# Optimization experiments

Hardware: AMD Instinct MI355X
Metric: run time of the kernel (lower is better)

## Reference

```python
import jax, jax.numpy as jnp
import numpy as np

N_NODES = 30000
N_EDGES = 480000
N_GRAPHS = 512
NUM_NEIGHBORS = 3.8
DIM_SH = 16       # l=0..3 spherical harmonics
DIM_GATE_IN = 160 # 16x0e+16x0o + 8x0e+8x0o+8x0e+8x0o + 16x1o+16x1e
DIM_GATE_OUT = 128
DIM_OUT = 7       # 0o + 6x0e


def spherical_harmonics_l3(u):
    # real spherical harmonics l=0..3, 'component' normalization (|Y_l|^2 ~ 2l+1)
    x, y, z = u[:, 0], u[:, 1], u[:, 2]
    x2, y2, z2 = x * x, y * y, z * z
    sh = [
        jnp.ones_like(x),
        3 ** 0.5 * x, 3 ** 0.5 * y, 3 ** 0.5 * z,
        15 ** 0.5 * x * y, 15 ** 0.5 * y * z,
        (5 ** 0.5 / 2) * (3 * z2 - 1),
        15 ** 0.5 * x * z,
        (15 ** 0.5 / 2) * (x2 - y2),
        (35 / 8) ** 0.5 * y * (3 * x2 - y2),
        105 ** 0.5 * x * y * z,
        (21 / 8) ** 0.5 * y * (5 * z2 - 1),
        (7 ** 0.5 / 2) * z * (5 * z2 - 3),
        (21 / 8) ** 0.5 * x * (5 * z2 - 1),
        (105 ** 0.5 / 2) * z * (x2 - y2),
        (35 / 8) ** 0.5 * x * (x2 - y2),
    ]
    return jnp.stack(sh, axis=-1)  # [E, 16]


def radial_embed(r):
    # soft_one_hot_linspace(start=0.5, end=2.5, number=3, basis='smooth_finite', cutoff=True) * sqrt(3)
    values = jnp.array([0.5, 1.5, 2.5], dtype=r.dtype)
    u = r[:, None] - values          # step = 1.0
    d = u * u - 1.0
    c = 1.14136 * np.exp(2.0)
    emb = jnp.where(d < 0, c * jnp.exp(1.0 / jnp.where(d < 0, d, -1.0)), 0.0)
    return emb * 3 ** 0.5            # [E, 3]


def mlp(s, W1, W2):
    # FullyConnectedNet([3, 256, K], relu): no bias, fan-in normalized
    h = jax.nn.relu(s @ (W1 / 3 ** 0.5))
    return h @ (W2 / 256 ** 0.5)


def conv(nf, edge_src, edge_dst, sh, w, cg, n_nodes):
    # gather -> per-edge weighted CG bilinear product -> scatter-add
    xs = nf[edge_src]                      # [E, Din]
    K, Din, Dsh = cg.shape
    E = xs.shape[0]
    if Din * Dsh <= 512:
        outer = (xs[:, :, None] * sh[:, None, :]).reshape(E, Din * Dsh)
        ef = outer @ cg.reshape(K, Din * Dsh).T           # [E, K]
    else:
        t = jnp.einsum('ei,kij->ekj', xs, cg)             # [E, K, Dsh] (K small)
        ef = jnp.einsum('ekj,ej->ek', t, sh)
    ef = ef * w                                           # per-edge learned weights
    out = jax.ops.segment_sum(ef, edge_dst, num_segments=n_nodes)
    return out / NUM_NEIGHBORS ** 0.5


def gate(x):
    # Gate('16x0e+16x0o', [relu, abs], '8x0e+8x0o+8x0e+8x0o', [relu,tanh,relu,tanh], '16x1o+16x1e')
    n = x.shape[0]
    s = jnp.concatenate([jax.nn.relu(x[:, :16]), jnp.abs(x[:, 16:32])], axis=1)
    g = jnp.concatenate([
        jax.nn.relu(x[:, 32:40]), jnp.tanh(x[:, 40:48]),
        jax.nn.relu(x[:, 48:56]), jnp.tanh(x[:, 56:64]),
    ], axis=1)                                            # [n, 32]
    vec = x[:, 64:160].reshape(n, 32, 3)                  # 16x1o + 16x1e
    gated = (vec * g[:, :, None]).reshape(n, 96)
    return jnp.concatenate([s, gated], axis=1)            # [n, 128]


def setup_inputs() -> dict:
    key = jax.random.key(0)
    ks = jax.random.split(key, 10)
    pos = jax.random.normal(ks[0], (N_NODES, 3), dtype=jnp.float32)
    edge_src = jax.random.randint(ks[1], (N_EDGES,), 0, N_NODES)
    edge_dst = jax.random.randint(ks[2], (N_EDGES,), 0, N_NODES)
    batch = jnp.sort(jax.random.randint(ks[3], (N_NODES,), 0, N_GRAPHS))
    W1a = jax.random.normal(ks[4], (3, 256), dtype=jnp.float32)
    W2a = jax.random.normal(ks[5], (256, DIM_GATE_IN), dtype=jnp.float32)
    cg1 = jax.random.normal(ks[6], (DIM_GATE_IN, DIM_SH, DIM_SH), dtype=jnp.float32) / DIM_SH
    W1b = jax.random.normal(ks[7], (3, 256), dtype=jnp.float32)
    W2b = jax.random.normal(ks[8], (256, DIM_OUT), dtype=jnp.float32)
    cg2 = jax.random.normal(ks[9], (DIM_OUT, DIM_GATE_OUT, DIM_SH), dtype=jnp.float32) / DIM_SH
    return {"pos": pos, "W1a": W1a, "W2a": W2a, "cg1": cg1, "W1b": W1b,
            "W2b": W2b, "cg2": cg2, "edge_src": edge_src, "edge_dst": edge_dst,
            "batch": batch}


def reference(pos, W1a, W2a, cg1, W1b, W2b, cg2, edge_src, edge_dst, batch):
    ev = pos[edge_src] - pos[edge_dst]                    # [E, 3]
    r = jnp.linalg.norm(ev, axis=1)
    u = ev / jnp.maximum(r, 1e-9)[:, None]
    sh = spherical_harmonics_l3(u)                        # [E, 16]
    scal = radial_embed(r)                                # [E, 3]

    # initial node features: scatter of edge attributes
    x = jax.ops.segment_sum(sh, edge_dst, num_segments=N_NODES) / NUM_NEIGHBORS ** 0.5

    w1 = mlp(scal, W1a, W2a)                              # [E, 160]
    x = conv(x, edge_src, edge_dst, sh, w1, cg1, N_NODES) # [N, 160]
    x = gate(x)                                           # [N, 128]
    w2 = mlp(scal, W1b, W2b)                              # [E, 7]
    x = conv(x, edge_src, edge_dst, sh, w2, cg2, N_NODES) # [N, 7]

    out = jax.ops.segment_sum(x, batch, num_segments=N_GRAPHS) / 4 ** 0.5
    return out                                            # [512, 7]
```

## Files before the change

### kernel.cpp

```cpp
#include <hip/hip_runtime.h>
#include <math.h>

#define NN 30000
#define NE 480000
#define NG 512

#define INV_SQRT_NN 0.5129891760425771f
#define INV_SQRT3   0.5773502691896258f
#define SCALE_W2    0.0625f
#define RAD_C       14.607377f

typedef __bf16 bf16x8 __attribute__((ext_vector_type(8)));
typedef float f32x4 __attribute__((ext_vector_type(4)));
typedef unsigned short ushort8 __attribute__((ext_vector_type(8)));

__device__ __forceinline__ unsigned short f2bf(float f) {
  unsigned int u = __float_as_uint(f);
  return (unsigned short)((u + 0x7FFFu + ((u >> 16) & 1u)) >> 16);
}

__global__ __launch_bounds__(256) void k_edge(
    const float* __restrict__ pos,
    const int* __restrict__ esrc,
    const int* __restrict__ edst,
    float* __restrict__ shg,
    float* __restrict__ scalg,
    float* __restrict__ x0) {
  __shared__ float S_lds[256*17];
  __shared__ int   d_lds[256];
  const int t = threadIdx.x;
  const int e = blockIdx.x * 256 + t;
  int s = esrc[e], d = edst[e];
  float ex = pos[3*s]   - pos[3*d];
  float ey = pos[3*s+1] - pos[3*d+1];
  float ez = pos[3*s+2] - pos[3*d+2];
  float r = sqrtf(ex*ex + ey*ey + ez*ez);
  float inv = 1.0f / fmaxf(r, 1e-9f);
  float x = ex*inv, y = ey*inv, z = ez*inv;
  float x2 = x*x, y2 = y*y, z2 = z*z;
  float S[16];
  S[0]  = 1.0f;
  S[1]  = 1.7320508075688772f * x;
  S[2]  = 1.7320508075688772f * y;
  S[3]  = 1.7320508075688772f * z;
  S[4]  = 3.872983346207417f * x * y;
  S[5]  = 3.872983346207417f * y * z;
  S[6]  = 1.118033988749895f * (3.0f*z2 - 1.0f);
  S[7]  = 3.872983346207417f * x * z;
  S[8]  = 1.9364916731037085f * (x2 - y2);
  S[9]  = 2.091650066335189f  * y * (3.0f*x2 - y2);
  S[10] = 10.246950765959598f * x * y * z;
  S[11] = 1.6201851746019651f * y * (5.0f*z2 - 1.0f);
  S[12] = 1.3228756555322954f * z * (5.0f*z2 - 3.0f);
  S[13] = 1.6201851746019651f * x * (5.0f*z2 - 1.0f);
  S[14] = 5.123475382979799f  * z * (x2 - y2);
  S[15] = 2.091650066335189f  * x * (x2 - y2);
  float4* shv = (float4*)(shg + (size_t)e * 16);
  shv[0] = make_float4(S[0],  S[1],  S[2],  S[3]);
  shv[1] = make_float4(S[4],  S[5],  S[6],  S[7]);
  shv[2] = make_float4(S[8],  S[9],  S[10], S[11]);
  shv[3] = make_float4(S[12], S[13], S[14], S[15]);
  float sc[3];
  #pragma unroll
  for (int c = 0; c < 3; ++c) {
    float v = 0.5f + (float)c;
    float uu = r - v;
    float dd = uu*uu - 1.0f;
    sc[c] = (dd < 0.0f) ? RAD_C * expf(1.0f/dd) : 0.0f;
  }
  ((float4*)scalg)[e] = make_float4(sc[0], sc[1], sc[2], 0.0f);

  d_lds[t] = d;
  #pragma unroll
  for (int j = 0; j < 16; ++j) S_lds[t*17 + j] = S[j];
  __syncthreads();
  #pragma unroll
  for (int it = 0; it < 16; ++it) {
    int idx = it*256 + t;
    int el = idx >> 4, j = idx & 15;
    atomicAdd(&x0[(size_t)d_lds[el]*16 + j], S_lds[el*17 + j]);
  }
}

__global__ void k_prep(const float* __restrict__ W2a, const float* __restrict__ cg1,
                       const float* __restrict__ cg2, const float* __restrict__ W2b,
                       unsigned short* __restrict__ Bcg, unsigned short* __restrict__ Bw2,
                       unsigned short* __restrict__ Bc2, unsigned short* __restrict__ Bw2b) {
  int tid = blockIdx.x * 256 + threadIdx.x;
  if (tid >= 12544) return;
  if (tid < 10240) {
    int sel = tid >= 5120;
    int t = sel ? tid - 5120 : tid;
    int lane = t & 63;
    int kc = (t >> 6) & 7;
    int nt = t >> 9;
    int n  = nt*16 + (lane & 15);
    int kb = kc*32 + (lane >> 4)*8;
    ushort8 v;
    if (!sel) {
      #pragma unroll
      for (int j = 0; j < 8; ++j) v[j] = f2bf(cg1[n*256 + kb + j]);
      *(ushort8*)&Bcg[(size_t)t*8] = v;
    } else {
      #pragma unroll
      for (int j = 0; j < 8; ++j) v[j] = f2bf(W2a[(kb + j)*160 + n] * SCALE_W2);
      *(ushort8*)&Bw2[(size_t)t*8] = v;
    }
  } else if (tid < 12032) {
    int et = tid - 10240;
    int L = et & 63;
    int kc = (et >> 6) & 3;
    int nt = et >> 8;
    int mcol = L & 15;
    int ib = kc*32 + (L >> 4)*8;
    ushort8 v;
    #pragma unroll
    for (int jj = 0; jj < 8; ++jj) v[jj] = f2bf(cg2[nt*2048 + (ib + jj)*16 + mcol]);
    *(ushort8*)&Bc2[(size_t)et*8] = v;
  } else {
    int et = tid - 12032;
    int L = et & 63;
    int kc = et >> 6;
    int mcol = L & 15;
    int ib = kc*32 + (L >> 4)*8;
    ushort8 v;
    #pragma unroll
    for (int jj = 0; jj < 8; ++jj)
      v[jj] = (mcol < 7) ? f2bf(W2b[(ib + jj)*7 + mcol] * SCALE_W2) : (unsigned short)0;
    *(ushort8*)&Bw2b[(size_t)et*8] = v;
  }
}

__global__ __launch_bounds__(256, 2) void k_conv1(
    const float* __restrict__ x0, const float* __restrict__ shg,
    const float* __restrict__ scalg,
    const int* __restrict__ esrc, const int* __restrict__ edst,
    const float* __restrict__ W1a,
    const unsigned short* __restrict__ Bcg, const unsigned short* __restrict__ Bw2,
    float* __restrict__ x1) {
  __shared__ float sh_lds[64*20];
  __shared__ float xs_lds[64*20];
  const int t = threadIdx.x;
  const int e0 = blockIdx.x * 64;

  {
    int e = t >> 2, q = t & 3;
    int ge = e0 + e;
    *(float4*)&sh_lds[e*20 + q*4] = ((const float4*)shg)[(size_t)ge*4 + q];
    float4 xv = ((const float4*)x0)[(size_t)esrc[ge]*4 + q];
    xv.x *= INV_SQRT_NN; xv.y *= INV_SQRT_NN; xv.z *= INV_SQRT_NN; xv.w *= INV_SQRT_NN;
    *(float4*)&xs_lds[e*20 + q*4] = xv;
  }
  const int L  = t & 63;
  const int wv = t >> 6;
  const int m  = L & 15;
  const int q4 = L >> 4;
  const int j0 = (q4 & 1) * 8;
  const int p  = q4 >> 1;
  const int el = wv*16 + m;

  float4 sc = ((const float4*)scalg)[e0 + el];
  const float hs0 = sc.x*INV_SQRT3, hs1 = sc.y*INV_SQRT3, hs2 = sc.z*INV_SQRT3;

  __syncthreads();
  float sh8[8];
  *(float4*)&sh8[0] = *(float4*)&sh_lds[el*20 + j0];
  *(float4*)&sh8[4] = *(float4*)&sh_lds[el*20 + j0 + 4];
  float xsc[8];
  #pragma unroll
  for (int kc = 0; kc < 8; ++kc) xsc[kc] = xs_lds[el*20 + kc*2 + p];

  f32x4 ac[10], aw[10];
  #pragma unroll
  for (int i = 0; i < 10; ++i) {
    ac[i] = (f32x4)(0.0f);
    aw[i] = (f32x4)(0.0f);
  }

  #pragma unroll
  for (int kc = 0; kc < 8; ++kc) {
    float xc = xsc[kc];
    ushort8 ao;
    #pragma unroll
    for (int j = 0; j < 8; ++j) ao[j] = f2bf(xc * sh8[j]);
    int mh = kc*32 + q4*8;
    float4 w0a = *(const float4*)&W1a[mh];
    float4 w0b = *(const float4*)&W1a[mh + 4];
    float4 w1a = *(const float4*)&W1a[256 + mh];
    float4 w1b = *(const float4*)&W1a[256 + mh + 4];
    float4 w2a = *(const float4*)&W1a[512 + mh];
    float4 w2b = *(const float4*)&W1a[512 + mh + 4];
    ushort8 ah;
    ah[0] = f2bf(fmaxf(hs0*w0a.x + hs1*w1a.x + hs2*w2a.x, 0.0f));
    ah[1] = f2bf(fmaxf(hs0*w0a.y + hs1*w1a.y + hs2*w2a.y, 0.0f));
    ah[2] = f2bf(fmaxf(hs0*w0a.z + hs1*w1a.z + hs2*w2a.z, 0.0f));
    ah[3] = f2bf(fmaxf(hs0*w0a.w + hs1*w1a.w + hs2*w2a.w, 0.0f));
    ah[4] = f2bf(fmaxf(hs0*w0b.x + hs1*w1b.x + hs2*w2b.x, 0.0f));
    ah[5] = f2bf(fmaxf(hs0*w0b.y + hs1*w1b.y + hs2*w2b.y, 0.0f));
    ah[6] = f2bf(fmaxf(hs0*w0b.z + hs1*w1b.z + hs2*w2b.z, 0.0f));
    ah[7] = f2bf(fmaxf(hs0*w0b.w + hs1*w1b.w + hs2*w2b.w, 0.0f));
    bf16x8 aoB = __builtin_bit_cast(bf16x8, ao);
    bf16x8 ahB = __builtin_bit_cast(bf16x8, ah);
    #pragma unroll
    for (int nt = 0; nt < 10; ++nt) {
      size_t bidx = (((size_t)nt*8 + kc)*64 + L)*8;
      ushort8 b1 = *(const ushort8*)&Bcg[bidx];
      ushort8 b2 = *(const ushort8*)&Bw2[bidx];
      ac[nt] = __builtin_amdgcn_mfma_f32_16x16x32_bf16(aoB, __builtin_bit_cast(bf16x8, b1), ac[nt], 0, 0, 0);
      aw[nt] = __builtin_amdgcn_mfma_f32_16x16x32_bf16(ahB, __builtin_bit_cast(bf16x8, b2), aw[nt], 0, 0, 0);
    }
  }

  int ebase = e0 + wv*16 + q4*4;
  int d0 = edst[ebase], d1 = edst[ebase+1], d2 = edst[ebase+2], d3 = edst[ebase+3];
  #pragma unroll
  for (int nt = 0; nt < 10; ++nt) {
    int col = nt*16 + m;
    atomicAdd(&x1[(size_t)d0*160 + col], ac[nt][0]*aw[nt][0]*INV_SQRT_NN);
    atomicAdd(&x1[(size_t)d1*160 + col], ac[nt][1]*aw[nt][1]*INV_SQRT_NN);
    atomicAdd(&x1[(size_t)d2*160 + col], ac[nt][2]*aw[nt][2]*INV_SQRT_NN);
    atomicAdd(&x1[(size_t)d3*160 + col], ac[nt][3]*aw[nt][3]*INV_SQRT_NN);
  }
}

__device__ __forceinline__ float gate_val(const float* xr, int o) {
  if (o < 16) return fmaxf(xr[o], 0.0f);
  if (o < 32) return fabsf(xr[o]);
  int oo = o - 32;
  int vi = oo / 3;
  float g = xr[32 + vi];
  g = (vi & 8) ? tanhf(g) : fmaxf(g, 0.0f);
  return xr[64 + oo] * g;
}

__global__ void k_gate(const float* __restrict__ x1, unsigned short* __restrict__ x2b) {
  int tid = blockIdx.x * 256 + threadIdx.x;
  if (tid >= NN*64) return;
  int n = tid >> 6, o2 = (tid & 63) * 2;
  const float* xr = x1 + (size_t)n * 160;
  ushort2 st;
  st.x = f2bf(gate_val(xr, o2));
  st.y = f2bf(gate_val(xr, o2 + 1));
  *(ushort2*)&x2b[(size_t)n*128 + o2] = st;
}

__global__ __launch_bounds__(256, 4) void k_conv2(
    const unsigned short* __restrict__ x2b, const float* __restrict__ shg,
    const float* __restrict__ scalg,
    const int* __restrict__ esrc, const int* __restrict__ edst,
    const float* __restrict__ W1b,
    const unsigned short* __restrict__ Bc2, const unsigned short* __restrict__ Bw2b,
    float* __restrict__ x3) {
  __shared__ float sh_lds[64*20];
  const int t = threadIdx.x;
  const int e0 = blockIdx.x * 64;
  {
    int e = t >> 2, q = t & 3;
    *(float4*)&sh_lds[e*20 + q*4] = ((const float4*)shg)[(size_t)(e0 + e)*4 + q];
  }
  __syncthreads();

  const int L = t & 63, wv = t >> 6;
  const int m = L & 15, q4 = L >> 4;
  const int el = wv*16 + m;
  const int ge = e0 + el;
  const int s_el = esrc[ge];
  float4 sc = ((const float4*)scalg)[ge];
  const float hs0 = sc.x*INV_SQRT3, hs1 = sc.y*INV_SQRT3, hs2 = sc.z*INV_SQRT3;

  f32x4 tAcc[7];
  #pragma unroll
  for (int nt = 0; nt < 7; ++nt) tAcc[nt] = (f32x4)(0.0f);
  f32x4 wAcc = (f32x4)(0.0f);

  const unsigned short* arow = x2b + (size_t)s_el*128 + q4*8;
  #pragma unroll
  for (int kc = 0; kc < 4; ++kc) {
    ushort8 a = *(const ushort8*)&arow[kc*32];
    bf16x8 aB = __builtin_bit_cast(bf16x8, a);
    #pragma unroll
    for (int nt = 0; nt < 7; ++nt) {
      ushort8 b = *(const ushort8*)&Bc2[(((size_t)nt*4 + kc)*64 + L)*8];
      tAcc[nt] = __builtin_amdgcn_mfma_f32_16x16x32_bf16(aB, __builtin_bit_cast(bf16x8, b), tAcc[nt], 0, 0, 0);
    }
  }
  #pragma unroll
  for (int kc = 0; kc < 8; ++kc) {
    int mh = kc*32 + q4*8;
    float4 w0a = *(const float4*)&W1b[mh];
    float4 w0b = *(const float4*)&W1b[mh + 4];
    float4 w1a = *(const float4*)&W1b[256 + mh];
    float4 w1b = *(const float4*)&W1b[256 + mh + 4];
    float4 w2a = *(const float4*)&W1b[512 + mh];
    float4 w2b = *(const float4*)&W1b[512 + mh + 4];
    ushort8 ah;
    ah[0] = f2bf(fmaxf(hs0*w0a.x + hs1*w1a.x + hs2*w2a.x, 0.0f));
    ah[1] = f2bf(fmaxf(hs0*w0a.y + hs1*w1a.y + hs2*w2a.y, 0.0f));
    ah[2] = f2bf(fmaxf(hs0*w0a.z + hs1*w1a.z + hs2*w2a.z, 0.0f));
    ah[3] = f2bf(fmaxf(hs0*w0a.w + hs1*w1a.w + hs2*w2a.w, 0.0f));
    ah[4] = f2bf(fmaxf(hs0*w0b.x + hs1*w1b.x + hs2*w2b.x, 0.0f));
    ah[5] = f2bf(fmaxf(hs0*w0b.y + hs1*w1b.y + hs2*w2b.y, 0.0f));
    ah[6] = f2bf(fmaxf(hs0*w0b.z + hs1*w1b.z + hs2*w2b.z, 0.0f));
    ah[7] = f2bf(fmaxf(hs0*w0b.w + hs1*w1b.w + hs2*w2b.w, 0.0f));
    ushort8 b = *(const ushort8*)&Bw2b[((size_t)kc*64 + L)*8];
    wAcc = __builtin_amdgcn_mfma_f32_16x16x32_bf16(
        __builtin_bit_cast(bf16x8, ah), __builtin_bit_cast(bf16x8, b), wAcc, 0, 0, 0);
  }

  int dsts[4];
  #pragma unroll
  for (int r = 0; r < 4; ++r) dsts[r] = edst[e0 + wv*16 + q4*4 + r];
  float ef[4] = {0.f, 0.f, 0.f, 0.f};
  #pragma unroll
  for (int nt = 0; nt < 7; ++nt) {
    #pragma unroll
    for (int r = 0; r < 4; ++r) {
      float v = tAcc[nt][r] * sh_lds[(wv*16 + q4*4 + r)*20 + m];
      v += __shfl_xor(v, 1);
      v += __shfl_xor(v, 2);
      v += __shfl_xor(v, 4);
      v += __shfl_xor(v, 8);
      if (m == nt) ef[r] = v;
    }
  }
  if (m < 7) {
    #pragma unroll
    for (int r = 0; r < 4; ++r)
      atomicAdd(&x3[(size_t)dsts[r]*7 + m], ef[r] * wAcc[r] * INV_SQRT_NN);
  }
}

__global__ void k_out(const float* __restrict__ x3, const int* __restrict__ batch,
                      float* __restrict__ out) {
  int tid = blockIdx.x * 256 + threadIdx.x;
  if (tid >= NN*7) return;
  int n = tid / 7;
  int k = tid - n*7;
  atomicAdd(&out[batch[n]*7 + k], x3[tid] * 0.5f);
}

extern "C" void kernel_launch(void* const* d_in, const int* in_sizes, int n_in,
                              void* d_out, int out_size, void* d_ws, size_t ws_size,
                              hipStream_t stream) {
  const float* pos  = (const float*)d_in[0];
  const float* W1a  = (const float*)d_in[1];
  const float* W2a  = (const float*)d_in[2];
  const float* cg1  = (const float*)d_in[3];
  const float* W1b  = (const float*)d_in[4];
  const float* W2b  = (const float*)d_in[5];
  const float* cg2  = (const float*)d_in[6];
  const int* esrc   = (const int*)d_in[7];
  const int* edst   = (const int*)d_in[8];
  const int* batch  = (const int*)d_in[9];
  float* out = (float*)d_out;

  float* ws    = (float*)d_ws;
  float* shg   = ws;
  float* scalg = shg   + (size_t)NE*16;
  float* x0    = scalg + (size_t)NE*4;
  float* x1    = x0    + (size_t)NN*16;
  float* x2g   = x1    + (size_t)NN*160;
  float* x3    = x2g   + (size_t)NN*128;
  unsigned short* x2b  = (unsigned short*)x2g;
  unsigned short* Bcg  = (unsigned short*)(x3 + (size_t)NN*7);
  unsigned short* Bw2  = Bcg + 40960;
  unsigned short* Bc2  = Bw2 + 40960;
  unsigned short* Bw2b = Bc2 + 14336;

  hipMemsetAsync(x0, 0, sizeof(float)*(size_t)NN*16, stream);
  hipMemsetAsync(x1, 0, sizeof(float)*(size_t)NN*160, stream);
  hipMemsetAsync(x3, 0, sizeof(float)*(size_t)NN*7, stream);
  hipMemsetAsync(d_out, 0, sizeof(float)*NG*7, stream);

  k_prep <<<49, 256, 0, stream>>>(W2a, cg1, cg2, W2b, Bcg, Bw2, Bc2, Bw2b);
  k_edge <<<NE/256, 256, 0, stream>>>(pos, esrc, edst, shg, scalg, x0);
  k_conv1<<<NE/64, 256, 0, stream>>>(x0, shg, scalg, esrc, edst, W1a, Bcg, Bw2, x1);
  k_gate <<<(NN*64)/256, 256, 0, stream>>>(x1, x2b);
  k_conv2<<<NE/64, 256, 0, stream>>>(x2b, shg, scalg, esrc, edst, W1b, Bc2, Bw2b, x3);
  k_out  <<<(NN*7 + 255)/256, 256, 0, stream>>>(x3, batch, out);
}
```

Baseline: 529.4 us.

## Process two 16-edge M-tiles per wave in conv1 to reuse B fragments

Each wave in k_conv1 now handles 32 edges (two 16-row MFMA tiles) instead of 16, so each B-operand fragment loaded from global (Bcg, Bw2) and the W1a rows feed twice as many MFMAs. Block size stays 256 threads but covers 128 edges, halving the grid. The gain is less global/L2 traffic per edge for the weight fragments. The cost is doubled accumulator registers (80 f32x4), which may lower occupancy or cause spills under the launch bound of 2 blocks per CU.

```diff
diff --git a/kernel.cpp b/kernel.cpp
--- a/kernel.cpp
+++ b/kernel.cpp
@@ -138,13 +138,15 @@
     const float* __restrict__ W1a,
     const unsigned short* __restrict__ Bcg, const unsigned short* __restrict__ Bw2,
     float* __restrict__ x1) {
-  __shared__ float sh_lds[64*20];
-  __shared__ float xs_lds[64*20];
+  __shared__ float sh_lds[128*20];
+  __shared__ float xs_lds[128*20];
   const int t = threadIdx.x;
-  const int e0 = blockIdx.x * 64;
-
-  {
-    int e = t >> 2, q = t & 3;
+  const int e0 = blockIdx.x * 128;
+
+  #pragma unroll
+  for (int i = 0; i < 2; ++i) {
+    int idx = t + 256*i;
+    int e = idx >> 2, q = idx & 3;
     int ge = e0 + e;
     *(float4*)&sh_lds[e*20 + q*4] = ((const float4*)shg)[(size_t)ge*4 + q];
     float4 xv = ((const float4*)x0)[(size_t)esrc[ge]*4 + q];
@@ -157,32 +159,40 @@
   const int q4 = L >> 4;
   const int j0 = (q4 & 1) * 8;
   const int p  = q4 >> 1;
-  const int el = wv*16 + m;
-
-  float4 sc = ((const float4*)scalg)[e0 + el];
-  const float hs0 = sc.x*INV_SQRT3, hs1 = sc.y*INV_SQRT3, hs2 = sc.z*INV_SQRT3;
+  const int el0 = wv*32 + m;
+  const int el1 = el0 + 16;
+
+  float4 scA = ((const float4*)scalg)[e0 + el0];
+  float4 scB = ((const float4*)scalg)[e0 + el1];
+  const float hsA0 = scA.x*INV_SQRT3, hsA1 = scA.y*INV_SQRT3, hsA2 = scA.z*INV_SQRT3;
+  const float hsB0 = scB.x*INV_SQRT3, hsB1 = scB.y*INV_SQRT3, hsB2 = scB.z*INV_SQRT3;
 
   __syncthreads();
-  float sh8[8];
-  *(float4*)&sh8[0] = *(float4*)&sh_lds[el*20 + j0];
-  *(float4*)&sh8[4] = *(float4*)&sh_lds[el*20 + j0 + 4];
-  float xsc[8];
-  #pragma unroll
-  for (int kc = 0; kc < 8; ++kc) xsc[kc] = xs_lds[el*20 + kc*2 + p];
-
-  f32x4 ac[10], aw[10];
-  #pragma unroll
-  for (int i = 0; i < 10; ++i) {
-    ac[i] = (f32x4)(0.0f);
-    aw[i] = (f32x4)(0.0f);
-  }
+  float sh8A[8], sh8B[8];
+  *(float4*)&sh8A[0] = *(float4*)&sh_lds[el0*20 + j0];
+  *(float4*)&sh8A[4] = *(float4*)&sh_lds[el0*20 + j0 + 4];
+  *(float4*)&sh8B[0] = *(float4*)&sh_lds[el1*20 + j0];
+  *(float4*)&sh8B[4] = *(float4*)&sh_lds[el1*20 + j0 + 4];
+
+  f32x4 ac[2][10], aw[2][10];
+  #pragma unroll
+  for (int mt = 0; mt < 2; ++mt)
+    #pragma unroll
+    for (int i = 0; i < 10; ++i) {
+      ac[mt][i] = (f32x4)(0.0f);
+      aw[mt][i] = (f32x4)(0.0f);
+    }
 
   #pragma unroll
   for (int kc = 0; kc < 8; ++kc) {
-    float xc = xsc[kc];
-    ushort8 ao;
-    #pragma unroll
-    for (int j = 0; j < 8; ++j) ao[j] = f2bf(xc * sh8[j]);
+    float xcA = xs_lds[el0*20 + kc*2 + p];
+    float xcB = xs_lds[el1*20 + kc*2 + p];
+    ushort8 aoA, aoB;
+    #pragma unroll
+    for (int j = 0; j < 8; ++j) {
+      aoA[j] = f2bf(xcA * sh8A[j]);
+      aoB[j] = f2bf(xcB * sh8B[j]);
+    }
     int mh = kc*32 + q4*8;
     float4 w0a = *(const float4*)&W1a[mh];
     float4 w0b = *(const float4*)&W1a[mh + 4];
@@ -190,36 +200,53 @@
     float4 w1b = *(const float4*)&W1a[256 + mh + 4];
     float4 w2a = *(const float4*)&W1a[512 + mh];
     float4 w2b = *(const float4*)&W1a[512 + mh + 4];
-    ushort8 ah;
-    ah[0] = f2bf(fmaxf(hs0*w0a.x + hs1*w1a.x + hs2*w2a.x, 0.0f));
-    ah[1] = f2bf(fmaxf(hs0*w0a.y + hs1*w1a.y + hs2*w2a.y, 0.0f));
-    ah[2] = f2bf(fmaxf(hs0*w0a.z + hs1*w1a.z + hs2*w2a.z, 0.0f));
-    ah[3] = f2bf(fmaxf(hs0*w0a.w + hs1*w1a.w + hs2*w2a.w, 0.0f));
-    ah[4] = f2bf(fmaxf(hs0*w0b.x + hs1*w1b.x + hs2*w2b.x, 0.0f));
-    ah[5] = f2bf(fmaxf(hs0*w0b.y + hs1*w1b.y + hs2*w2b.y, 0.0f));
-    ah[6] = f2bf(fmaxf(hs0*w0b.z + hs1*w1b.z + hs2*w2b.z, 0.0f));
-    ah[7] = f2bf(fmaxf(hs0*w0b.w + hs1*w1b.w + hs2*w2b.w, 0.0f));
-    bf16x8 aoB = __builtin_bit_cast(bf16x8, ao);
-    bf16x8 ahB = __builtin_bit_cast(bf16x8, ah);
+    ushort8 ahA, ahB;
+    ahA[0] = f2bf(fmaxf(hsA0*w0a.x + hsA1*w1a.x + hsA2*w2a.x, 0.0f));
+    ahA[1] = f2bf(fmaxf(hsA0*w0a.y + hsA1*w1a.y + hsA2*w2a.y, 0.0f));
+    ahA[2] = f2bf(fmaxf(hsA0*w0a.z + hsA1*w1a.z + hsA2*w2a.z, 0.0f));
+    ahA[3] = f2bf(fmaxf(hsA0*w0a.w + hsA1*w1a.w + hsA2*w2a.w, 0.0f));
+    ahA[4] = f2bf(fmaxf(hsA0*w0b.x + hsA1*w1b.x + hsA2*w2b.x, 0.0f));
+    ahA[5] = f2bf(fmaxf(hsA0*w0b.y + hsA1*w1b.y + hsA2*w2b.y, 0.0f));
+    ahA[6] = f2bf(fmaxf(hsA0*w0b.z + hsA1*w1b.z + hsA2*w2b.z, 0.0f));
+    ahA[7] = f2bf(fmaxf(hsA0*w0b.w + hsA1*w1b.w + hsA2*w2b.w, 0.0f));
+    ahB[0] = f2bf(fmaxf(hsB0*w0a.x + hsB1*w1a.x + hsB2*w2a.x, 0.0f));
+    ahB[1] = f2bf(fmaxf(hsB0*w0a.y + hsB1*w1a.y + hsB2*w2a.y, 0.0f));
+    ahB[2] = f2bf(fmaxf(hsB0*w0a.z + hsB1*w1a.z + hsB2*w2a.z, 0.0f));
+    ahB[3] = f2bf(fmaxf(hsB0*w0a.w + hsB1*w1a.w + hsB2*w2a.w, 0.0f));
+    ahB[4] = f2bf(fmaxf(hsB0*w0b.x + hsB1*w1b.x + hsB2*w2b.x, 0.0f));
+    ahB[5] = f2bf(fmaxf(hsB0*w0b.y + hsB1*w1b.y + hsB2*w2b.y, 0.0f));
+    ahB[6] = f2bf(fmaxf(hsB0*w0b.z + hsB1*w1b.z + hsB2*w2b.z, 0.0f));
+    ahB[7] = f2bf(fmaxf(hsB0*w0b.w + hsB1*w1b.w + hsB2*w2b.w, 0.0f));
+    bf16x8 aoAB = __builtin_bit_cast(bf16x8, aoA);
+    bf16x8 aoBB = __builtin_bit_cast(bf16x8, aoB);
+    bf16x8 ahAB = __builtin_bit_cast(bf16x8, ahA);
+    bf16x8 ahBB = __builtin_bit_cast(bf16x8, ahB);
     #pragma unroll
     for (int nt = 0; nt < 10; ++nt) {
       size_t bidx = (((size_t)nt*8 + kc)*64 + L)*8;
       ushort8 b1 = *(const ushort8*)&Bcg[bidx];
       ushort8 b2 = *(const ushort8*)&Bw2[bidx];
-      ac[nt] = __builtin_amdgcn_mfma_f32_16x16x32_bf16(aoB, __builtin_bit_cast(bf16x8, b1), ac[nt], 0, 0, 0);
-      aw[nt] = __builtin_amdgcn_mfma_f32_16x16x32_bf16(ahB, __builtin_bit_cast(bf16x8, b2), aw[nt], 0, 0, 0);
-    }
-  }
-
-  int ebase = e0 + wv*16 + q4*4;
-  int d0 = edst[ebase], d1 = edst[ebase+1], d2 = edst[ebase+2], d3 = edst[ebase+3];
-  #pragma unroll
-  for (int nt = 0; nt < 10; ++nt) {
-    int col = nt*16 + m;
-    atomicAdd(&x1[(size_t)d0*160 + col], ac[nt][0]*aw[nt][0]*INV_SQRT_NN);
-    atomicAdd(&x1[(size_t)d1*160 + col], ac[nt][1]*aw[nt][1]*INV_SQRT_NN);
-    atomicAdd(&x1[(size_t)d2*160 + col], ac[nt][2]*aw[nt][2]*INV_SQRT_NN);
-    atomicAdd(&x1[(size_t)d3*160 + col], ac[nt][3]*aw[nt][3]*INV_SQRT_NN);
+      bf16x8 b1B = __builtin_bit_cast(bf16x8, b1);
+      bf16x8 b2B = __builtin_bit_cast(bf16x8, b2);
+      ac[0][nt] = __builtin_amdgcn_mfma_f32_16x16x32_bf16(aoAB, b1B, ac[0][nt], 0, 0, 0);
+      ac[1][nt] = __builtin_amdgcn_mfma_f32_16x16x32_bf16(aoBB, b1B, ac[1][nt], 0, 0, 0);
+      aw[0][nt] = __builtin_amdgcn_mfma_f32_16x16x32_bf16(ahAB, b2B, aw[0][nt], 0, 0, 0);
+      aw[1][nt] = __builtin_amdgcn_mfma_f32_16x16x32_bf16(ahBB, b2B, aw[1][nt], 0, 0, 0);
+    }
+  }
+
+  #pragma unroll
+  for (int mt = 0; mt < 2; ++mt) {
+    int ebase = e0 + wv*32 + mt*16 + q4*4;
+    int d0 = edst[ebase], d1 = edst[ebase+1], d2 = edst[ebase+2], d3 = edst[ebase+3];
+    #pragma unroll
+    for (int nt = 0; nt < 10; ++nt) {
+      int col = nt*16 + m;
+      atomicAdd(&x1[(size_t)d0*160 + col], ac[mt][nt][0]*aw[mt][nt][0]*INV_SQRT_NN);
+      atomicAdd(&x1[(size_t)d1*160 + col], ac[mt][nt][1]*aw[mt][nt][1]*INV_SQRT_NN);
+      atomicAdd(&x1[(size_t)d2*160 + col], ac[mt][nt][2]*aw[mt][nt][2]*INV_SQRT_NN);
+      atomicAdd(&x1[(size_t)d3*160 + col], ac[mt][nt][3]*aw[mt][nt][3]*INV_SQRT_NN);
+    }
   }
 }
 
@@ -374,7 +401,7 @@
 
   k_prep <<<49, 256, 0, stream>>>(W2a, cg1, cg2, W2b, Bcg, Bw2, Bc2, Bw2b);
   k_edge <<<NE/256, 256, 0, stream>>>(pos, esrc, edst, shg, scalg, x0);
-  k_conv1<<<NE/64, 256, 0, stream>>>(x0, shg, scalg, esrc, edst, W1a, Bcg, Bw2, x1);
+  k_conv1<<<NE/128, 256, 0, stream>>>(x0, shg, scalg, esrc, edst, W1a, Bcg, Bw2, x1);
   k_gate <<<(NN*64)/256, 256, 0, stream>>>(x1, x2b);
   k_conv2<<<NE/64, 256, 0, stream>>>(x2b, shg, scalg, esrc, edst, W1b, Bc2, Bw2b, x3);
   k_out  <<<(NN*7 + 255)/256, 256, 0, stream>>>(x3, batch, out);
```

Measured after the change: 601.5 us. 1.14x slower.

## Split conv1 waves into CG-product and radial-MLP roles exchanged through LDS

Applied to the files above, without the earlier changes.

Restructures the first convolution kernel so that two waves compute the CG bilinear MFMAs and the other two compute the radial MLP weight MFMAs. Each wave now covers all 64 edges and half of the output columns. Each B fragment is loaded once per kc and reused across four M tiles, which cuts repeated global loads of Bcg/Bw2. The MLP waves pass their accumulators through a large LDS buffer (about 42 KB), and the CG waves then multiply and issue the atomics. This adds an extra barrier, raises LDS use (which may cut occupancy under launch_bounds(256,2)), and leaves half the waves idle during the atomic phase.

```diff
diff --git a/kernel.cpp b/kernel.cpp
--- a/kernel.cpp
+++ b/kernel.cpp
@@ -140,6 +140,7 @@
     float* __restrict__ x1) {
   __shared__ float sh_lds[64*20];
   __shared__ float xs_lds[64*20];
+  __shared__ unsigned long long wacc_u64[2*64*41];
   const int t = threadIdx.x;
   const int e0 = blockIdx.x * 64;
 
@@ -157,69 +158,113 @@
   const int q4 = L >> 4;
   const int j0 = (q4 & 1) * 8;
   const int p  = q4 >> 1;
-  const int el = wv*16 + m;
-
-  float4 sc = ((const float4*)scalg)[e0 + el];
-  const float hs0 = sc.x*INV_SQRT3, hs1 = sc.y*INV_SQRT3, hs2 = sc.z*INV_SQRT3;
-
+  const int slot = wv & 1;
+
+  f32x4 acc[4][5];
+  #pragma unroll
+  for (int mt = 0; mt < 4; ++mt)
+    #pragma unroll
+    for (int n = 0; n < 5; ++n) acc[mt][n] = (f32x4)(0.0f);
+
+  if (wv < 2) {
+    __syncthreads();
+    float sh8[4][8];
+    #pragma unroll
+    for (int mt = 0; mt < 4; ++mt) {
+      int el = mt*16 + m;
+      *(float4*)&sh8[mt][0] = *(float4*)&sh_lds[el*20 + j0];
+      *(float4*)&sh8[mt][4] = *(float4*)&sh_lds[el*20 + j0 + 4];
+    }
+    #pragma unroll
+    for (int kc = 0; kc < 8; ++kc) {
+      ushort8 ao[4];
+      #pragma unroll
+      for (int mt = 0; mt < 4; ++mt) {
+        float xc = xs_lds[(mt*16 + m)*20 + kc*2 + p];
+        #pragma unroll
+        for (int j = 0; j < 8; ++j) ao[mt][j] = f2bf(xc * sh8[mt][j]);
+      }
+      #pragma unroll
+      for (int ntl = 0; ntl < 5; ++ntl) {
+        size_t bidx = (((size_t)(slot*5 + ntl)*8 + kc)*64 + L)*8;
+        bf16x8 bB = __builtin_bit_cast(bf16x8, *(const ushort8*)&Bcg[bidx]);
+        #pragma unroll
+        for (int mt = 0; mt < 4; ++mt)
+          acc[mt][ntl] = __builtin_amdgcn_mfma_f32_16x16x32_bf16(
+              __builtin_bit_cast(bf16x8, ao[mt]), bB, acc[mt][ntl], 0, 0, 0);
+      }
+    }
+  } else {
+    float hs[4][3];
+    #pragma unroll
+    for (int mt = 0; mt < 4; ++mt) {
+      float4 sc = ((const float4*)scalg)[e0 + mt*16 + m];
+      hs[mt][0] = sc.x*INV_SQRT3; hs[mt][1] = sc.y*INV_SQRT3; hs[mt][2] = sc.z*INV_SQRT3;
+    }
+    __syncthreads();
+    #pragma unroll
+    for (int kc = 0; kc < 8; ++kc) {
+      int mh = kc*32 + q4*8;
+      float4 w0a = *(const float4*)&W1a[mh];
+      float4 w0b = *(const float4*)&W1a[mh + 4];
+      float4 w1a = *(const float4*)&W1a[256 + mh];
+      float4 w1b = *(const float4*)&W1a[256 + mh + 4];
+      float4 w2a = *(const float4*)&W1a[512 + mh];
+      float4 w2b = *(const float4*)&W1a[512 + mh + 4];
+      ushort8 ah[4];
+      #pragma unroll
+      for (int mt = 0; mt < 4; ++mt) {
+        float h0 = hs[mt][0], h1 = hs[mt][1], h2 = hs[mt][2];
+        ah[mt][0] = f2bf(fmaxf(h0*w0a.x + h1*w1a.x + h2*w2a.x, 0.0f));
+        ah[mt][1] = f2bf(fmaxf(h0*w0a.y + h1*w1a.y + h2*w2a.y, 0.0f));
+        ah[mt][2] = f2bf(fmaxf(h0*w0a.z + h1*w1a.z + h2*w2a.z, 0.0f));
+        ah[mt][3] = f2bf(fmaxf(h0*w0a.w + h1*w1a.w + h2*w2a.w, 0.0f));
+        ah[mt][4] = f2bf(fmaxf(h0*w0b.x + h1*w1b.x + h2*w2b.x, 0.0f));
+        ah[mt][5] = f2bf(fmaxf(h0*w0b.y + h1*w1b.y + h2*w2b.y, 0.0f));
+        ah[mt][6] = f2bf(fmaxf(h0*w0b.z + h1*w1b.z + h2*w2b.z, 0.0f));
+        ah[mt][7] = f2bf(fmaxf(h0*w0b.w + h1*w1b.w + h2*w2b.w, 0.0f));
+      }
+      #pragma unroll
+      for (int ntl = 0; ntl < 5; ++ntl) {
+        size_t bidx = (((size_t)(slot*5 + ntl)*8 + kc)*64 + L)*8;
+        bf16x8 bB = __builtin_bit_cast(bf16x8, *(const ushort8*)&Bw2[bidx]);
+        #pragma unroll
+        for (int mt = 0; mt < 4; ++mt)
+          acc[mt][ntl] = __builtin_amdgcn_mfma_f32_16x16x32_bf16(
+              __builtin_bit_cast(bf16x8, ah[mt]), bB, acc[mt][ntl], 0, 0, 0);
+      }
+    }
+    unsigned long long* wb = &wacc_u64[((size_t)slot*64 + L)*41];
+    #pragma unroll
+    for (int mt = 0; mt < 4; ++mt)
+      #pragma unroll
+      for (int ntl = 0; ntl < 5; ++ntl) {
+        float2 lo = make_float2(acc[mt][ntl][0], acc[mt][ntl][1]);
+        float2 hi = make_float2(acc[mt][ntl][2], acc[mt][ntl][3]);
+        wb[(mt*5 + ntl)*2 + 0] = *(unsigned long long*)&lo;
+        wb[(mt*5 + ntl)*2 + 1] = *(unsigned long long*)&hi;
+      }
+  }
   __syncthreads();
-  float sh8[8];
-  *(float4*)&sh8[0] = *(float4*)&sh_lds[el*20 + j0];
-  *(float4*)&sh8[4] = *(float4*)&sh_lds[el*20 + j0 + 4];
-  float xsc[8];
-  #pragma unroll
-  for (int kc = 0; kc < 8; ++kc) xsc[kc] = xs_lds[el*20 + kc*2 + p];
-
-  f32x4 ac[10], aw[10];
-  #pragma unroll
-  for (int i = 0; i < 10; ++i) {
-    ac[i] = (f32x4)(0.0f);
-    aw[i] = (f32x4)(0.0f);
-  }
-
-  #pragma unroll
-  for (int kc = 0; kc < 8; ++kc) {
-    float xc = xsc[kc];
-    ushort8 ao;
-    #pragma unroll
-    for (int j = 0; j < 8; ++j) ao[j] = f2bf(xc * sh8[j]);
-    int mh = kc*32 + q4*8;
-    float4 w0a = *(const float4*)&W1a[mh];
-    float4 w0b = *(const float4*)&W1a[mh + 4];
-    float4 w1a = *(const float4*)&W1a[256 + mh];
-    float4 w1b = *(const float4*)&W1a[256 + mh + 4];
-    float4 w2a = *(const float4*)&W1a[512 + mh];
-    float4 w2b = *(const float4*)&W1a[512 + mh + 4];
-    ushort8 ah;
-    ah[0] = f2bf(fmaxf(hs0*w0a.x + hs1*w1a.x + hs2*w2a.x, 0.0f));
-    ah[1] = f2bf(fmaxf(hs0*w0a.y + hs1*w1a.y + hs2*w2a.y, 0.0f));
-    ah[2] = f2bf(fmaxf(hs0*w0a.z + hs1*w1a.z + hs2*w2a.z, 0.0f));
-    ah[3] = f2bf(fmaxf(hs0*w0a.w + hs1*w1a.w + hs2*w2a.w, 0.0f));
-    ah[4] = f2bf(fmaxf(hs0*w0b.x + hs1*w1b.x + hs2*w2b.x, 0.0f));
-    ah[5] = f2bf(fmaxf(hs0*w0b.y + hs1*w1b.y + hs2*w2b.y, 0.0f));
-    ah[6] = f2bf(fmaxf(hs0*w0b.z + hs1*w1b.z + hs2*w2b.z, 0.0f));
-    ah[7] = f2bf(fmaxf(hs0*w0b.w + hs1*w1b.w + hs2*w2b.w, 0.0f));
-    bf16x8 aoB = __builtin_bit_cast(bf16x8, ao);
-    bf16x8 ahB = __builtin_bit_cast(bf16x8, ah);
-    #pragma unroll
-    for (int nt = 0; nt < 10; ++nt) {
-      size_t bidx = (((size_t)nt*8 + kc)*64 + L)*8;
-      ushort8 b1 = *(const ushort8*)&Bcg[bidx];
-      ushort8 b2 = *(const ushort8*)&Bw2[bidx];
-      ac[nt] = __builtin_amdgcn_mfma_f32_16x16x32_bf16(aoB, __builtin_bit_cast(bf16x8, b1), ac[nt], 0, 0, 0);
-      aw[nt] = __builtin_amdgcn_mfma_f32_16x16x32_bf16(ahB, __builtin_bit_cast(bf16x8, b2), aw[nt], 0, 0, 0);
-    }
-  }
-
-  int ebase = e0 + wv*16 + q4*4;
-  int d0 = edst[ebase], d1 = edst[ebase+1], d2 = edst[ebase+2], d3 = edst[ebase+3];
-  #pragma unroll
-  for (int nt = 0; nt < 10; ++nt) {
-    int col = nt*16 + m;
-    atomicAdd(&x1[(size_t)d0*160 + col], ac[nt][0]*aw[nt][0]*INV_SQRT_NN);
-    atomicAdd(&x1[(size_t)d1*160 + col], ac[nt][1]*aw[nt][1]*INV_SQRT_NN);
-    atomicAdd(&x1[(size_t)d2*160 + col], ac[nt][2]*aw[nt][2]*INV_SQRT_NN);
-    atomicAdd(&x1[(size_t)d3*160 + col], ac[nt][3]*aw[nt][3]*INV_SQRT_NN);
+  if (wv < 2) {
+    const unsigned long long* wb = &wacc_u64[((size_t)slot*64 + L)*41];
+    #pragma unroll
+    for (int mt = 0; mt < 4; ++mt) {
+      int ebase = e0 + mt*16 + q4*4;
+      int d0 = edst[ebase], d1 = edst[ebase+1], d2 = edst[ebase+2], d3 = edst[ebase+3];
+      #pragma unroll
+      for (int ntl = 0; ntl < 5; ++ntl) {
+        unsigned long long plo = wb[(mt*5 + ntl)*2 + 0];
+        unsigned long long phi = wb[(mt*5 + ntl)*2 + 1];
+        float2 lo = *(float2*)&plo;
+        float2 hi = *(float2*)&phi;
+        int col = (slot*5 + ntl)*16 + m;
+        atomicAdd(&x1[(size_t)d0*160 + col], acc[mt][ntl][0]*lo.x*INV_SQRT_NN);
+        atomicAdd(&x1[(size_t)d1*160 + col], acc[mt][ntl][1]*lo.y*INV_SQRT_NN);
+        atomicAdd(&x1[(size_t)d2*160 + col], acc[mt][ntl][2]*hi.x*INV_SQRT_NN);
+        atomicAdd(&x1[(size_t)d3*160 + col], acc[mt][ntl][3]*hi.y*INV_SQRT_NN);
+      }
+    }
   }
 }
 
```

Result: slower. 588.0 us (+11.1%).

## Stage B-operand panels through double-buffered LDS with register prefetch in conv1

Applied to the files above, without the earlier changes.

In k_conv1 each of the four waves used to fetch every B fragment (Bcg and Bw2) for all 10 column tiles straight from global memory, so every wave loaded the same weights. The blocked B panels are now split across waves, staged cooperatively into a double-buffered shared-memory area, and the next k-chunk is prefetched into registers while the MFMAs for the current chunk run. This removes the redundant global/L2 traffic per wave but adds 40KB of LDS per block, a barrier per k-chunk and more register pressure, which may reduce occupancy under launch_bounds(256,2).

```diff
diff --git a/kernel.cpp b/kernel.cpp
--- a/kernel.cpp
+++ b/kernel.cpp
@@ -140,6 +140,7 @@
     float* __restrict__ x1) {
   __shared__ float sh_lds[64*20];
   __shared__ float xs_lds[64*20];
+  __shared__ unsigned short Bpan[2][20*512];
   const int t = threadIdx.x;
   const int e0 = blockIdx.x * 64;
 
@@ -159,10 +160,27 @@
   const int p  = q4 >> 1;
   const int el = wv*16 + m;
 
+  const unsigned short* psrc[5];
+  unsigned short* pdst0[5];
+  #pragma unroll
+  for (int i = 0; i < 5; ++i) {
+    int pnl = wv*5 + i;
+    int g = pnl >= 10;
+    int nt = g ? pnl - 10 : pnl;
+    psrc[i] = (g ? Bw2 : Bcg) + (((size_t)nt*8)*64 + L)*8;
+    pdst0[i] = &Bpan[0][pnl*512 + L*8];
+  }
+
   float4 sc = ((const float4*)scalg)[e0 + el];
   const float hs0 = sc.x*INV_SQRT3, hs1 = sc.y*INV_SQRT3, hs2 = sc.z*INV_SQRT3;
 
+  ushort8 pf[5];
+  #pragma unroll
+  for (int i = 0; i < 5; ++i) pf[i] = *(const ushort8*)psrc[i];
+  #pragma unroll
+  for (int i = 0; i < 5; ++i) *(ushort8*)pdst0[i] = pf[i];
   __syncthreads();
+
   float sh8[8];
   *(float4*)&sh8[0] = *(float4*)&sh_lds[el*20 + j0];
   *(float4*)&sh8[4] = *(float4*)&sh_lds[el*20 + j0 + 4];
@@ -179,6 +197,10 @@
 
   #pragma unroll
   for (int kc = 0; kc < 8; ++kc) {
+    if (kc < 7) {
+      #pragma unroll
+      for (int i = 0; i < 5; ++i) pf[i] = *(const ushort8*)(psrc[i] + (size_t)(kc+1)*512);
+    }
     float xc = xsc[kc];
     ushort8 ao;
     #pragma unroll
@@ -201,13 +223,19 @@
     ah[7] = f2bf(fmaxf(hs0*w0b.w + hs1*w1b.w + hs2*w2b.w, 0.0f));
     bf16x8 aoB = __builtin_bit_cast(bf16x8, ao);
     bf16x8 ahB = __builtin_bit_cast(bf16x8, ah);
+    const unsigned short* buf = &Bpan[kc & 1][0];
     #pragma unroll
     for (int nt = 0; nt < 10; ++nt) {
-      size_t bidx = (((size_t)nt*8 + kc)*64 + L)*8;
-      ushort8 b1 = *(const ushort8*)&Bcg[bidx];
-      ushort8 b2 = *(const ushort8*)&Bw2[bidx];
+      ushort8 b1 = *(const ushort8*)&buf[nt*512 + L*8];
+      ushort8 b2 = *(const ushort8*)&buf[(10 + nt)*512 + L*8];
       ac[nt] = __builtin_amdgcn_mfma_f32_16x16x32_bf16(aoB, __builtin_bit_cast(bf16x8, b1), ac[nt], 0, 0, 0);
       aw[nt] = __builtin_amdgcn_mfma_f32_16x16x32_bf16(ahB, __builtin_bit_cast(bf16x8, b2), aw[nt], 0, 0, 0);
+    }
+    if (kc < 7) {
+      unsigned short* dst = &Bpan[(kc + 1) & 1][0];
+      #pragma unroll
+      for (int i = 0; i < 5; ++i) *(ushort8*)(dst + (wv*5 + i)*512 + L*8) = pf[i];
+      __syncthreads();
     }
   }
 
```

Result: faster. 498.7 us (-5.8%).
